# Kernel tuning notes

Measured on AMD Instinct MI355X. Metric: run time of the kernel, lower is better.

## Reference

```python
import jax, jax.numpy as jnp
import numpy as np

MAX_DISP = 4  # max_displacement
PAD = MAX_DISP
ODIM = 2 * MAX_DISP + 1  # 9 -> 81 cost-volume channels


def setup_inputs() -> dict:
    key = jax.random.key(0)
    k1, k2 = jax.random.split(key)
    B, C, H, W = 4, 256, 96, 192
    x1 = jax.random.normal(k1, (B, C, H, W), dtype=jnp.float32)
    x2 = jax.random.normal(k2, (B, C, H, W), dtype=jnp.float32)
    return {"x1": x1, "x2": x2}


def reference(x1, x2):
    B, C, H, W = x1.shape
    # zero-pad x2 spatially by PAD on each side (matches F.pad([pad]*4))
    x2p = jnp.pad(x2, ((0, 0), (0, 0), (PAD, PAD), (PAD, PAD)))
    cv = []
    for i in range(ODIM):          # fixed 9x9 displacement grid
        for j in range(ODIM):
            shifted = jax.lax.dynamic_slice(
                x2p, (0, 0, i, j), (B, C, H, W))
            # mean over channel dim -> [B, H, W]
            cv.append(jnp.mean(x1 * shifted, axis=1))
    return jnp.stack(cv, axis=1)  # [B, 81, H, W]
```

## Files before the change

kernel.cpp:

```cpp
#include <hip/hip_runtime.h>
#include <stddef.h>


#define NB 4
#define NC 256
#define HH 96
#define WW 192
#define TW 16
#define TH 4
#define KC 32
#define NROWS 12
#define CHW (HH * WW)
#define KSTRIDE (KC * CHW)
#define NTASK 1152

#define XT_ELEMS (NB * HH * WW * NC)
#define XT_BYTES ((size_t)XT_ELEMS * 2)

#define WSTR 36
#define RSTR (24 * WSTR)
#define BUFSZ 10688

typedef __attribute__((ext_vector_type(8))) short bf16x8;
typedef __attribute__((ext_vector_type(4))) float f32x4;

__device__ __forceinline__ unsigned short f2bf(float f) {
    union { float f; unsigned u; } c; c.f = f;
    unsigned r = c.u + 0x7FFFu + ((c.u >> 16) & 1u);
    return (unsigned short)(r >> 16);
}

__global__ __launch_bounds__(256) void transpose_cast(
    const float* __restrict__ x1, const float* __restrict__ x2,
    unsigned short* __restrict__ xt1, unsigned short* __restrict__ xt2)
{
    __shared__ float t[64][65];
    int lin = blockIdx.x;
    const int wt = lin % 3; lin /= 3;
    const int ct = lin & 3; lin >>= 2;
    const int h  = lin % 96; lin /= 96;
    const int b  = lin & 3;  lin >>= 2;
    const float* __restrict__ src = lin ? x2 : x1;
    unsigned short* __restrict__ dst = lin ? xt2 : xt1;
    const int w0 = wt * 64, c0 = ct * 64;

    const int wi = threadIdx.x & 63, c4 = threadIdx.x >> 6;
#pragma unroll
    for (int it = 0; it < 16; ++it) {
        const int c = it * 4 + c4;
        t[c][wi] = src[((size_t)((b * NC + c0 + c) * HH + h)) * WW + w0 + wi];
    }
    __syncthreads();
    const int co = (threadIdx.x & 31) * 2, wo = threadIdx.x >> 5;
#pragma unroll
    for (int it = 0; it < 8; ++it) {
        const int w = it * 8 + wo;
        ushort2 v;
        v.x = f2bf(t[co][w]);
        v.y = f2bf(t[co + 1][w]);
        *(ushort2*)&dst[((size_t)((b * HH + h) * WW + w0 + w)) * NC + c0 + co] = v;
    }
}

__global__ __launch_bounds__(512, 4) void corr_mfma_bt(
    const unsigned short* __restrict__ xt1,
    const unsigned short* __restrict__ xt2,
    float* __restrict__ out)
{
    __shared__ union {
        unsigned short xb[2 * BUFSZ];
        float band[TH][9][9][18];
    } lds;

    const int lin = blockIdx.x;
    const int sw  = (lin & 7) * 144 + (lin >> 3);
    const int b   = sw / 288;
    const int t2  = sw - b * 288;
    const int ty  = t2 / 12;
    const int tx  = t2 - ty * 12;

    const int tid  = threadIdx.x;
    const int wv   = tid >> 6;
    const int lane = tid & 63;
    const int col  = lane & 15;
    const int q    = lane >> 4;
    const int r    = wv & 3;
    const int dig  = wv >> 2;
    const int w0   = tx * TW;
    const int h0   = ty * TH;
    const int h    = h0 + r;

    f32x4 acc[9];
#pragma unroll
    for (int s = 0; s < 9; ++s) acc[s] = (f32x4)0.0f;

    unsigned go2[3];
    int      lof[3];
    bool     okk[3];
#pragma unroll
    for (int k = 0; k < 3; ++k) {
        const int g   = tid + k * 512;
        const bool act = (g < NTASK);
        const int row = g / 96;
        const int rem = g - row * 96;
        const int w   = rem >> 2;
        const int sub = rem & 3;
        const int gh  = h0 - 4 + row;
        const int gw  = w0 - 4 + w;
        const bool inb = (gh >= 0) & (gh < HH) & (gw >= 0) & (gw < WW);
        okk[k] = act & inb;
        const int ghc = gh < 0 ? 0 : (gh > HH - 1 ? HH - 1 : gh);
        const int gwc = gw < 0 ? 0 : (gw > WW - 1 ? WW - 1 : gw);
        const int rwc = row > NROWS - 1 ? NROWS - 1 : row;
        go2[k] = (unsigned)(((b * HH + ghc) * WW + gwc) * NC + sub * 8);
        lof[k] = rwc * RSTR + w * WSTR + sub * 8;
        if (act & !inb) {
            uint4 z = make_uint4(0, 0, 0, 0);
            *(uint4*)&lds.xb[lof[k]] = z;
            *(uint4*)&lds.xb[BUFSZ + lof[k]] = z;
        }
    }

    uint4 pfu[3];
#pragma unroll
    for (int k = 0; k < 3; ++k) {
        if (okk[k]) pfu[k] = *(const uint4*)&xt2[go2[k]];
        go2[k] += KC;
    }
    unsigned o1 = (unsigned)(((b * HH + h) * WW + w0 + col) * NC + q * 8);
    bf16x8 a_cur = *(const bf16x8*)&xt1[o1]; o1 += KC;
    bf16x8 a_nxt = a_cur;

    const int rb = r * RSTR + q * 8;

#pragma unroll
    for (int ci = 0; ci < 8; ++ci) {
        const int pb = (ci & 1) * BUFSZ;
#pragma unroll
        for (int k = 0; k < 3; ++k)
            if (okk[k]) *(uint4*)&lds.xb[pb + lof[k]] = pfu[k];
        if (ci < 7) {
#pragma unroll
            for (int k = 0; k < 3; ++k) {
                if (okk[k]) pfu[k] = *(const uint4*)&xt2[go2[k]];
                go2[k] += KC;
            }
            a_nxt = *(const bf16x8*)&xt1[o1]; o1 += KC;
        }
        __syncthreads();
#pragma unroll
        for (int s = 0; s < 9; ++s) {
            const int u  = dig * 9 + s;
            const int di = u >> 1;
            const int n  = (u & 1) * 16 + col;
            const bf16x8 bb = *(const bf16x8*)&lds.xb[pb + rb + di * RSTR + n * WSTR];
            acc[s] = __builtin_amdgcn_mfma_f32_16x16x32_bf16(a_cur, bb, acc[s], 0, 0, 0);
        }
        a_cur = a_nxt;
    }
    __syncthreads();

#pragma unroll
    for (int s = 0; s < 9; ++s) {
        const int u  = dig * 9 + s;
        const int di = u >> 1;
        const int uh = u & 1;
#pragma unroll
        for (int rg = 0; rg < 4; ++rg) {
            int m  = q * 4 + rg;
            int dj = uh * 16 + col - m;
            if (dj >= 0 && dj < 9)
                lds.band[r][di][dj][m] = acc[s][rg];
        }
    }
    __syncthreads();

    const float scale = 1.0f / 256.0f;
#pragma unroll
    for (int it = 0; it < 11; ++it) {
        int gi = it * 32 + (tid >> 4);
        if (gi < 324) {
            int combo = gi >> 2;
            int row   = gi & 3;
            float v = lds.band[row][combo / 9][combo % 9][tid & 15];
            out[((size_t)((b * 81 + combo) * HH + h0 + row)) * WW + w0 + (tid & 15)] = v * scale;
        }
    }
}

#define KS 264
#define RS 1096
#define XBI(row, kg, n) ((row) * RS + (kg) * KS + (n) * 8)

__global__ __launch_bounds__(512, 4) void corr_mfma_fb(
    const float* __restrict__ x1, const float* __restrict__ x2,
    float* __restrict__ out)
{
    __shared__ union {
        unsigned short xb[NROWS * RS];
        float band[TH][9][9][18];
    } lds;

    const int lin = blockIdx.x;
    const int sw  = (lin & 7) * 144 + (lin >> 3);
    const int b   = sw / 288;
    const int t2  = sw - b * 288;
    const int ty  = t2 / 12;
    const int tx  = t2 - ty * 12;

    const int tid  = threadIdx.x;
    const int wv   = tid >> 6;
    const int lane = tid & 63;
    const int col  = lane & 15;
    const int q    = lane >> 4;
    const int r    = wv & 3;
    const int dig  = wv >> 2;
    const int w0   = tx * TW;
    const int h0   = ty * TH;
    const int h    = h0 + r;

    f32x4 acc[9];
#pragma unroll
    for (int s = 0; s < 9; ++s) acc[s] = (f32x4)0.0f;

    unsigned o2k[3];
    int      lofk[3];
    bool     okk[3];
    bool     act[3];
#pragma unroll
    for (int k = 0; k < 3; ++k) {
        const int t   = tid + k * 512;
        act[k] = (t < NTASK);
        const int seg = t % 6;
        const int u   = t / 6;
        const int cp  = u & 15;
        const int row = u >> 4;
        const int gh  = h0 - 4 + row;
        const int gw  = w0 - 4 + seg * 4;
        okk[k] = act[k] & (gh >= 0) & (gh < HH) & (gw >= 0) & (gw <= WW - 4);
        const int ghc = gh < 0 ? 0 : (gh > HH - 1 ? HH - 1 : gh);
        const int gwc = gw < 0 ? 0 : gw;
        const int rwc = row > NROWS - 1 ? NROWS - 1 : row;
        o2k[k]  = (unsigned)(((b * NC + cp * 2) * HH + ghc) * WW + gwc);
        lofk[k] = XBI(rwc, cp >> 2, seg * 4) + (cp & 3) * 2;
    }
    unsigned o1 = (unsigned)(((b * NC + q * 8) * HH + h) * WW + w0 + col);

    float pf[24];
    float pa[8];

#define STAGE_LOAD_FB()                                                  \
    {                                                                    \
        _Pragma("unroll")                                                \
        for (int k = 0; k < 3; ++k) {                                    \
            _Pragma("unroll")                                            \
            for (int e = 0; e < 2; ++e) {                                \
                float4 ld = make_float4(0.f, 0.f, 0.f, 0.f);             \
                if (okk[k]) ld = *(const float4*)&x2[o2k[k] + e * CHW];  \
                *(float4*)&pf[(k * 2 + e) * 4] = ld;                     \
            }                                                            \
            o2k[k] += KSTRIDE;                                           \
        }                                                                \
    }

#define X1_LOAD_FB()                                                     \
    {                                                                    \
        _Pragma("unroll")                                                \
        for (int j = 0; j < 8; ++j) pa[j] = x1[o1 + j * CHW];            \
        o1 += KSTRIDE;                                                   \
    }

    STAGE_LOAD_FB();
    X1_LOAD_FB();

    const int rbase = XBI(r, q, col);

    for (int ci = 0; ci < 8; ++ci) {
#pragma unroll
        for (int k = 0; k < 3; ++k) {
            if (act[k]) {
#pragma unroll
                for (int p = 0; p < 4; ++p) {
                    ushort2 v;
                    v.x = f2bf(pf[(k * 2 + 0) * 4 + p]);
                    v.y = f2bf(pf[(k * 2 + 1) * 4 + p]);
                    *(ushort2*)&lds.xb[lofk[k] + p * 8] = v;
                }
            }
        }
        __syncthreads();

        bf16x8 a;
#pragma unroll
        for (int j = 0; j < 8; ++j) a[j] = (short)f2bf(pa[j]);
        if (ci < 7) {
            STAGE_LOAD_FB();
            X1_LOAD_FB();
        }

#pragma unroll
        for (int s = 0; s < 9; ++s) {
            const int u    = dig * 9 + s;
            const int di   = u >> 1;
            const int half = u & 1;
            bf16x8 bb = *(const bf16x8*)&lds.xb[rbase + di * RS + half * 128];
            acc[s] = __builtin_amdgcn_mfma_f32_16x16x32_bf16(a, bb, acc[s], 0, 0, 0);
        }
        __syncthreads();
    }

#pragma unroll
    for (int s = 0; s < 9; ++s) {
        const int u  = dig * 9 + s;
        const int di = u >> 1;
        const int uh = u & 1;
#pragma unroll
        for (int rg = 0; rg < 4; ++rg) {
            int m  = q * 4 + rg;
            int dj = uh * 16 + col - m;
            if (dj >= 0 && dj < 9)
                lds.band[r][di][dj][m] = acc[s][rg];
        }
    }
    __syncthreads();

    const float scale = 1.0f / 256.0f;
#pragma unroll
    for (int it = 0; it < 11; ++it) {
        int gi = it * 32 + (tid >> 4);
        if (gi < 324) {
            int combo = gi >> 2;
            int row   = gi & 3;
            float v = lds.band[row][combo / 9][combo % 9][tid & 15];
            out[((size_t)((b * 81 + combo) * HH + h0 + row)) * WW + w0 + (tid & 15)] = v * scale;
        }
    }
}

extern "C" void kernel_launch(void* const* d_in, const int* in_sizes, int n_in,
                              void* d_out, int out_size, void* d_ws, size_t ws_size,
                              hipStream_t stream) {
    const float* x1 = (const float*)d_in[0];
    const float* x2 = (const float*)d_in[1];
    float* out = (float*)d_out;

    if (ws_size >= 2 * XT_BYTES) {
        unsigned short* xt1 = (unsigned short*)d_ws;
        unsigned short* xt2 = xt1 + XT_ELEMS;
        transpose_cast<<<dim3(9216), 256, 0, stream>>>(x1, x2, xt1, xt2);
        corr_mfma_bt<<<dim3(1152), 512, 0, stream>>>(xt1, xt2, out);
    } else {
        corr_mfma_fb<<<dim3(1152), 512, 0, stream>>>(x1, x2, out);
    }
}
```

Before: 261.5 us.

## Pre-pad x2 in global memory and read MFMA operands directly, skip x1 transpose

Only x2 is transposed to a zero-padded channels-last bf16 buffer; a separate kernel zeroes the pad border. The correlation kernel drops the LDS staging and double buffering and loads B fragments straight from global memory (relying on L1/L2 reuse across the nine displacement rows). It also reads x1 in its original NCHW fp32 layout and converts to bf16 in registers. This removes the x1 transpose pass and the LDS barriers, at the cost of redundant global loads, more register pressure (launch bounds lowered to 2 blocks per CU) and an extra launch.

```diff
diff --git a/kernel.cpp b/kernel.cpp
--- a/kernel.cpp
+++ b/kernel.cpp
@@ -9,17 +9,14 @@
 #define TW 16
 #define TH 4
 #define KC 32
-#define NROWS 12
 #define CHW (HH * WW)
-#define KSTRIDE (KC * CHW)
-#define NTASK 1152
-
-#define XT_ELEMS (NB * HH * WW * NC)
-#define XT_BYTES ((size_t)XT_ELEMS * 2)
-
-#define WSTR 36
-#define RSTR (24 * WSTR)
-#define BUFSZ 10688
+
+#define HP 104
+#define WP 208
+#define PROW (WP * NC)
+#define PIMG (HP * PROW)
+#define XT2_ELEMS (NB * PIMG)
+#define XT2_BYTES ((size_t)XT2_ELEMS * 2)
 
 typedef __attribute__((ext_vector_type(8))) short bf16x8;
 typedef __attribute__((ext_vector_type(4))) float f32x4;
@@ -30,47 +27,75 @@
     return (unsigned short)(r >> 16);
 }
 
-__global__ __launch_bounds__(256) void transpose_cast(
-    const float* __restrict__ x1, const float* __restrict__ x2,
-    unsigned short* __restrict__ xt1, unsigned short* __restrict__ xt2)
+#define NTOP (NB * 8 * WP * 32)
+#define NSIDE (NB * HH * 16 * 32)
+__global__ __launch_bounds__(256) void pad_zero(unsigned short* __restrict__ xt2p)
+{
+    const uint4 z = make_uint4(0, 0, 0, 0);
+    int t = blockIdx.x * 256 + threadIdx.x;
+    const int stride = gridDim.x * 256;
+    for (; t < NTOP + NSIDE; t += stride) {
+        unsigned e;
+        if (t < NTOP) {
+            const int cg = t & 31;
+            const int w  = (t >> 5) % WP;
+            const int rr = (t >> 5) / WP;
+            const int b  = rr >> 3;
+            const int hh = rr & 7;
+            const int hp = hh < 4 ? hh : 96 + hh;
+            e = (unsigned)((b * HP + hp) * WP + w) * NC + cg * 8;
+        } else {
+            const int u  = t - NTOP;
+            const int cg = u & 31;
+            const int ws = (u >> 5) & 15;
+            const int rr = (u >> 5) >> 4;
+            const int b  = rr / HH;
+            const int hp = 4 + rr % HH;
+            const int wp = ws < 4 ? ws : 192 + ws;
+            e = (unsigned)((b * HP + hp) * WP + wp) * NC + cg * 8;
+        }
+        *(uint4*)&xt2p[e] = z;
+    }
+}
+
+__global__ __launch_bounds__(256) void transpose_x2(
+    const float* __restrict__ x2, unsigned short* __restrict__ xt2p)
 {
     __shared__ float t[64][65];
     int lin = blockIdx.x;
     const int wt = lin % 3; lin /= 3;
     const int ct = lin & 3; lin >>= 2;
     const int h  = lin % 96; lin /= 96;
-    const int b  = lin & 3;  lin >>= 2;
-    const float* __restrict__ src = lin ? x2 : x1;
-    unsigned short* __restrict__ dst = lin ? xt2 : xt1;
+    const int b  = lin & 3;
     const int w0 = wt * 64, c0 = ct * 64;
 
     const int wi = threadIdx.x & 63, c4 = threadIdx.x >> 6;
 #pragma unroll
     for (int it = 0; it < 16; ++it) {
         const int c = it * 4 + c4;
-        t[c][wi] = src[((size_t)((b * NC + c0 + c) * HH + h)) * WW + w0 + wi];
+        t[c][wi] = x2[((size_t)((b * NC + c0 + c) * HH + h)) * WW + w0 + wi];
     }
     __syncthreads();
-    const int co = (threadIdx.x & 31) * 2, wo = threadIdx.x >> 5;
-#pragma unroll
-    for (int it = 0; it < 8; ++it) {
-        const int w = it * 8 + wo;
-        ushort2 v;
-        v.x = f2bf(t[co][w]);
-        v.y = f2bf(t[co + 1][w]);
-        *(ushort2*)&dst[((size_t)((b * HH + h) * WW + w0 + w)) * NC + c0 + co] = v;
-    }
-}
-
-__global__ __launch_bounds__(512, 4) void corr_mfma_bt(
-    const unsigned short* __restrict__ xt1,
-    const unsigned short* __restrict__ xt2,
+#pragma unroll
+    for (int it = 0; it < 2; ++it) {
+        const int task = it * 256 + threadIdx.x;
+        const int cg = task & 7;
+        const int w  = task >> 3;
+        bf16x8 v;
+#pragma unroll
+        for (int j = 0; j < 8; ++j) v[j] = (short)f2bf(t[cg * 8 + j][w]);
+        const unsigned e = (unsigned)((b * HP + h + 4) * WP + (w0 + 4 + w)) * NC
+                         + c0 + cg * 8;
+        *(bf16x8*)&xt2p[e] = v;
+    }
+}
+
+__global__ __launch_bounds__(512, 2) void corr_mfma_g(
+    const float* __restrict__ x1,
+    const unsigned short* __restrict__ xt2p,
     float* __restrict__ out)
 {
-    __shared__ union {
-        unsigned short xb[2 * BUFSZ];
-        float band[TH][9][9][18];
-    } lds;
+    __shared__ float band[TH][9][9][18];
 
     const int lin = blockIdx.x;
     const int sw  = (lin & 7) * 144 + (lin >> 3);
@@ -94,71 +119,40 @@
 #pragma unroll
     for (int s = 0; s < 9; ++s) acc[s] = (f32x4)0.0f;
 
-    unsigned go2[3];
-    int      lof[3];
-    bool     okk[3];
-#pragma unroll
-    for (int k = 0; k < 3; ++k) {
-        const int g   = tid + k * 512;
-        const bool act = (g < NTASK);
-        const int row = g / 96;
-        const int rem = g - row * 96;
-        const int w   = rem >> 2;
-        const int sub = rem & 3;
-        const int gh  = h0 - 4 + row;
-        const int gw  = w0 - 4 + w;
-        const bool inb = (gh >= 0) & (gh < HH) & (gw >= 0) & (gw < WW);
-        okk[k] = act & inb;
-        const int ghc = gh < 0 ? 0 : (gh > HH - 1 ? HH - 1 : gh);
-        const int gwc = gw < 0 ? 0 : (gw > WW - 1 ? WW - 1 : gw);
-        const int rwc = row > NROWS - 1 ? NROWS - 1 : row;
-        go2[k] = (unsigned)(((b * HH + ghc) * WW + gwc) * NC + sub * 8);
-        lof[k] = rwc * RSTR + w * WSTR + sub * 8;
-        if (act & !inb) {
-            uint4 z = make_uint4(0, 0, 0, 0);
-            *(uint4*)&lds.xb[lof[k]] = z;
-            *(uint4*)&lds.xb[BUFSZ + lof[k]] = z;
-        }
-    }
-
-    uint4 pfu[3];
-#pragma unroll
-    for (int k = 0; k < 3; ++k) {
-        if (okk[k]) pfu[k] = *(const uint4*)&xt2[go2[k]];
-        go2[k] += KC;
-    }
-    unsigned o1 = (unsigned)(((b * HH + h) * WW + w0 + col) * NC + q * 8);
-    bf16x8 a_cur = *(const bf16x8*)&xt1[o1]; o1 += KC;
-    bf16x8 a_nxt = a_cur;
-
-    const int rb = r * RSTR + q * 8;
-
-#pragma unroll
+    unsigned l2[9];
+#pragma unroll
+    for (int s = 0; s < 9; ++s) {
+        const int u    = dig * 9 + s;
+        const int di   = u >> 1;
+        const int n    = (u & 1) * 16 + col;
+        l2[s] = (unsigned)((b * HP + h + di) * WP + (w0 + n)) * NC + q * 8;
+    }
+    unsigned o1 = (unsigned)((b * NC + q * 8) * HH + h) * WW + w0 + col;
+
+    float pa[8];
+#pragma unroll
+    for (int j = 0; j < 8; ++j) pa[j] = x1[o1 + j * CHW];
+    o1 += KC * CHW;
+
     for (int ci = 0; ci < 8; ++ci) {
-        const int pb = (ci & 1) * BUFSZ;
-#pragma unroll
-        for (int k = 0; k < 3; ++k)
-            if (okk[k]) *(uint4*)&lds.xb[pb + lof[k]] = pfu[k];
+        bf16x8 bfr[9];
+#pragma unroll
+        for (int s = 0; s < 9; ++s) {
+            bfr[s] = *(const bf16x8*)&xt2p[l2[s]];
+            l2[s] += KC;
+        }
+        bf16x8 a;
+#pragma unroll
+        for (int j = 0; j < 8; ++j) a[j] = (short)f2bf(pa[j]);
         if (ci < 7) {
 #pragma unroll
-            for (int k = 0; k < 3; ++k) {
-                if (okk[k]) pfu[k] = *(const uint4*)&xt2[go2[k]];
-                go2[k] += KC;
-            }
-            a_nxt = *(const bf16x8*)&xt1[o1]; o1 += KC;
-        }
-        __syncthreads();
-#pragma unroll
-        for (int s = 0; s < 9; ++s) {
-            const int u  = dig * 9 + s;
-            const int di = u >> 1;
-            const int n  = (u & 1) * 16 + col;
-            const bf16x8 bb = *(const bf16x8*)&lds.xb[pb + rb + di * RSTR + n * WSTR];
-            acc[s] = __builtin_amdgcn_mfma_f32_16x16x32_bf16(a_cur, bb, acc[s], 0, 0, 0);
-        }
-        a_cur = a_nxt;
-    }
-    __syncthreads();
+            for (int j = 0; j < 8; ++j) pa[j] = x1[o1 + j * CHW];
+            o1 += KC * CHW;
+        }
+#pragma unroll
+        for (int s = 0; s < 9; ++s)
+            acc[s] = __builtin_amdgcn_mfma_f32_16x16x32_bf16(a, bfr[s], acc[s], 0, 0, 0);
+    }
 
 #pragma unroll
     for (int s = 0; s < 9; ++s) {
@@ -170,7 +164,7 @@
             int m  = q * 4 + rg;
             int dj = uh * 16 + col - m;
             if (dj >= 0 && dj < 9)
-                lds.band[r][di][dj][m] = acc[s][rg];
+                band[r][di][dj][m] = acc[s][rg];
         }
     }
     __syncthreads();
@@ -182,14 +176,17 @@
         if (gi < 324) {
             int combo = gi >> 2;
             int row   = gi & 3;
-            float v = lds.band[row][combo / 9][combo % 9][tid & 15];
+            float v = band[row][combo / 9][combo % 9][tid & 15];
             out[((size_t)((b * 81 + combo) * HH + h0 + row)) * WW + w0 + (tid & 15)] = v * scale;
         }
     }
 }
 
+#define NROWS 12
+#define NTASK 1152
 #define KS 264
 #define RS 1096
+#define KSTRIDE (KC * CHW)
 #define XBI(row, kg, n) ((row) * RS + (kg) * KS + (n) * 8)
 
 __global__ __launch_bounds__(512, 4) void corr_mfma_fb(
@@ -344,11 +341,11 @@
     const float* x2 = (const float*)d_in[1];
     float* out = (float*)d_out;
 
-    if (ws_size >= 2 * XT_BYTES) {
-        unsigned short* xt1 = (unsigned short*)d_ws;
-        unsigned short* xt2 = xt1 + XT_ELEMS;
-        transpose_cast<<<dim3(9216), 256, 0, stream>>>(x1, x2, xt1, xt2);
-        corr_mfma_bt<<<dim3(1152), 512, 0, stream>>>(xt1, xt2, out);
+    if (ws_size >= XT2_BYTES) {
+        unsigned short* xt2p = (unsigned short*)d_ws;
+        pad_zero<<<dim3(512), 256, 0, stream>>>(xt2p);
+        transpose_x2<<<dim3(4608), 256, 0, stream>>>(x2, xt2p);
+        corr_mfma_g<<<dim3(1152), 512, 0, stream>>>(x1, xt2p, out);
     } else {
         corr_mfma_fb<<<dim3(1152), 512, 0, stream>>>(x1, x2, out);
     }
```

After: 264.7 us. About the same (+1.2%).
